# Kernel optimization log

Measured on AMD Instinct MI355X. Metric: run time of the kernel, lower is better.

The kernel has to match this reference:

```python
import jax, jax.numpy as jnp
import numpy as np

B, T, C = 4, 1024, 1024
NH, L, DHR, FF = 16, 512, 64, 4096
DK = C // NH  # 64
EPS = 1e-6
NEG = -9e15


def rms_norm(x, w):
    var = jnp.mean(jnp.square(x), axis=-1, keepdims=True)
    return x * jax.lax.rsqrt(var + EPS) * w


def rope_apply(x):
    # Faithful to RoPE module: freq = t+1, pos pairs repeated, theta = exp(-2*pos/C*ln(1e4))
    b, t, c = x.shape
    xf = x.astype(jnp.float32)
    freq = jnp.arange(t, dtype=jnp.float32)[:, None] + 1.0           # [t,1]
    pos = jnp.arange(c // 2, dtype=jnp.float32)[:, None]
    pos = jnp.repeat(pos, 2, axis=-1).reshape(1, -1)                 # [1,c] -> p0,p0,p1,p1,...
    theta = jnp.exp(-2.0 * pos / c * jnp.log(10000.0))
    cos = jnp.cos(freq * theta)                                      # [t,c]
    sin = jnp.sin(freq * theta)
    x2 = xf.reshape(b, t, c // 2, 2)
    rot = jnp.stack([-x2[..., 1], x2[..., 0]], axis=-1).reshape(b, t, c)
    return (xf * cos + rot * sin).astype(x.dtype)


def setup_inputs() -> dict:
    key = jax.random.key(0)
    ks = jax.random.split(key, 12)
    s = 0.02
    return {
        "x": jax.random.normal(ks[0], (B, T, C), jnp.float32),
        "rms1": jnp.ones((C,), jnp.float32),
        "rms2": jnp.ones((C,), jnp.float32),
        "W_dkv": s * jax.random.normal(ks[1], (C, 2 * L), jnp.float32),
        "b_dkv": jnp.zeros((2 * L,), jnp.float32),
        "W_kr": s * jax.random.normal(ks[2], (2 * L, DHR), jnp.float32),
        "b_kr": jnp.zeros((DHR,), jnp.float32),
        "W_qr": s * jax.random.normal(ks[3], (2 * L, DHR * NH), jnp.float32),
        "b_qr": jnp.zeros((DHR * NH,), jnp.float32),
        "W_kv": s * jax.random.normal(ks[4], (L, 2 * C), jnp.float32),
        "b_kv": jnp.zeros((2 * C,), jnp.float32),
        "W_q": s * jax.random.normal(ks[5], (L, C), jnp.float32),
        "b_q": jnp.zeros((C,), jnp.float32),
        "W_o": s * jax.random.normal(ks[6], (C, C), jnp.float32),
        "b_o": jnp.zeros((C,), jnp.float32),
        "W_f1": s * jax.random.normal(ks[7], (C, FF), jnp.float32),
        "b_f1": jnp.zeros((FF,), jnp.float32),
        "W_f2": s * jax.random.normal(ks[8], (FF, C), jnp.float32),
        "b_f2": jnp.zeros((C,), jnp.float32),
    }


def mla(x, W_dkv, b_dkv, W_kr, b_kr, W_qr, b_qr, W_kv, b_kv, W_q, b_q, W_o, b_o):
    b, t, c = x.shape
    comp = jnp.einsum('btc,cd->btd', x, W_dkv) + b_dkv               # [B,T,2L]
    cKV, cq = jnp.split(comp, 2, axis=-1)                            # [B,T,L] each
    # RoPE branches (computed from the compressed representation, as in source)
    kR = rope_apply(jnp.einsum('btl,ld->btd', comp, W_kr) + b_kr)    # [B,T,DHR]
    qR = rope_apply(jnp.einsum('btl,ld->btd', comp, W_qr) + b_qr)    # roped over full NH*DHR dim
    qR = qR.reshape(b, t, NH, DHR).transpose(0, 2, 1, 3)             # [B,NH,T,DHR]
    kv = jnp.einsum('btl,ld->btd', cKV, W_kv) + b_kv
    k, v = jnp.split(kv, 2, axis=-1)                                 # [B,T,C] each
    q = jnp.einsum('btl,ld->btd', cq, W_q) + b_q                     # [B,T,C]
    to_heads = lambda z: z.reshape(b, t, NH, DK).transpose(0, 2, 1, 3)
    q, k, v = to_heads(q), to_heads(k), to_heads(v)                  # [B,NH,T,DK]
    q = jnp.concatenate([q, qR], axis=-1)                            # [B,NH,T,DK+DHR]
    k = jnp.concatenate([k, jnp.broadcast_to(kR[:, None], (b, NH, t, DHR))], axis=-1)
    # manual masked softmax in fp32, scale uses DK (not DK+DHR), faithful to source
    scale = 1.0 / np.sqrt(DK)
    w = jnp.einsum('bnqd,bnkd->bnqk', q.astype(jnp.float32), k.astype(jnp.float32)) * scale
    mask = jnp.tril(jnp.ones((t, t), jnp.float32))
    w = jnp.where(mask == 0, NEG, w)
    p = jax.nn.softmax(w, axis=-1)
    o = jnp.einsum('bnqk,bnkd->bnqd', p, v.astype(jnp.float32)).astype(x.dtype)
    o = o.transpose(0, 2, 1, 3).reshape(b, t, c)
    return jnp.einsum('btc,cd->btd', o, W_o) + b_o


def ffn(x, W_f1, b_f1, W_f2, b_f2):
    h = jax.nn.gelu(jnp.einsum('btc,cf->btf', x, W_f1) + b_f1)
    return jnp.einsum('btf,fc->btc', h, W_f2) + b_f2


def reference(x, rms1, rms2, W_dkv, b_dkv, W_kr, b_kr, W_qr, b_qr,
              W_kv, b_kv, W_q, b_q, W_o, b_o, W_f1, b_f1, W_f2, b_f2):
    h = x + mla(rms_norm(x, rms1), W_dkv, b_dkv, W_kr, b_kr, W_qr, b_qr,
                W_kv, b_kv, W_q, b_q, W_o, b_o)
    out = h + ffn(rms_norm(h, rms2), W_f1, b_f1, W_f2, b_f2)
    return out
```

## Files before the change

### kernel.cpp

```cpp
#include <hip/hip_runtime.h>

typedef unsigned int u32;
typedef unsigned short u16;
typedef __bf16 bf16x8 __attribute__((ext_vector_type(8)));
typedef float f32x4 __attribute__((ext_vector_type(4)));

#define B_ 4
#define T_ 1024
#define C_ 1024
#define NH_ 16
#define L_ 512
#define DHR_ 64
#define FF_ 4096

typedef __attribute__((address_space(3))) u32 as3_u32;
typedef __attribute__((address_space(1))) u32 as1_u32;

__device__ __forceinline__ void gld16(const u16* g, u16* l) {
  __builtin_amdgcn_global_load_lds((const as1_u32*)g, (as3_u32*)l, 16, 0, 0);
}

__device__ __forceinline__ float bf2f(u16 u) {
  union { u32 i; float f; } v; v.i = ((u32)u) << 16; return v.f;
}
__device__ __forceinline__ u16 f2bf(float f) {
  union { float f; u32 i; } v; v.f = f;
  u32 r = (v.i + 0x7FFFu + ((v.i >> 16) & 1u)) >> 16;
  return (u16)r;
}

__global__ void transpose_kernel(const float* __restrict__ in, u16* __restrict__ outp,
                                 int R, int C) {
  __shared__ float tile[32][33];
  int bx = blockIdx.x * 32;
  int by = blockIdx.y * 32;
  int tx = threadIdx.x, ty = threadIdx.y;
  for (int i = ty; i < 32; i += 8)
    tile[i][tx] = in[(size_t)(by + i) * C + bx + tx];
  __syncthreads();
  for (int i = ty; i < 32; i += 8)
    outp[(size_t)(bx + i) * R + by + tx] = f2bf(tile[tx][i]);
}

__global__ __launch_bounds__(256) void rmsnorm_kernel(const float* __restrict__ xin,
                                                      const float* __restrict__ w,
                                                      u16* __restrict__ outp) {
  const int row = blockIdx.x;
  const int tid = threadIdx.x;
  const float* xp = xin + (size_t)row * C_;
  float v[4];
#pragma unroll
  for (int i = 0; i < 4; i++) v[i] = xp[tid + 256 * i];
  float ss = v[0] * v[0] + v[1] * v[1] + v[2] * v[2] + v[3] * v[3];
#pragma unroll
  for (int o = 32; o > 0; o >>= 1) ss += __shfl_down(ss, o, 64);
  __shared__ float red[4];
  if ((tid & 63) == 0) red[tid >> 6] = ss;
  __syncthreads();
  ss = red[0] + red[1] + red[2] + red[3];
  float scale = rsqrtf(ss * (1.0f / 1024.0f) + 1e-6f);
  u16* op = outp + (size_t)row * C_;
#pragma unroll
  for (int i = 0; i < 4; i++)
    op[tid + 256 * i] = f2bf(v[i] * scale * w[tid + 256 * i]);
}

template<int EPI, bool NCLIP>
__device__ __forceinline__ void g128_body(
    u16* As, u16* Bs,
    const u16* __restrict__ A, int lda, int aoff,
    const u16* __restrict__ BT, const float* __restrict__ bias,
    const float* __restrict__ resid, void* __restrict__ out,
    int N, int Kfull, int Klen, int m0, int n0, int koff) {
  const int tid = threadIdx.x;
  const int wave = tid >> 6, lane = tid & 63;
  const int wm = wave >> 1, wn = wave & 1;
  const int quad = lane >> 4, l15 = lane & 15;
  const int row = tid >> 2, seg = tid & 3;

  const u16* aP = A + (size_t)(m0 + row) * lda + aoff + koff + seg * 8;
  const u16* bP = BT + (size_t)(n0 + row) * Kfull + koff + seg * 8;
  u16* aL = As + row * 32 + seg * 8;
  u16* bL = Bs + row * 32 + seg * 8;
  const size_t aStep = (size_t)64 * lda;
  const size_t bStep = (size_t)64 * Kfull;

  f32x4 acc[4][4] = {};

  for (int k0 = 0; k0 < Klen; k0 += 32) {
    gld16(aP + k0, aL);
    gld16(aP + k0 + aStep, aL + 64 * 32);
    gld16(bP + k0, bL);
    gld16(bP + k0 + bStep, bL + 64 * 32);
    __syncthreads();
    bf16x8 af[4], bf[4];
#pragma unroll
    for (int mt = 0; mt < 4; mt++)
      af[mt] = *(const bf16x8*)&As[(wm * 64 + mt * 16 + l15) * 32 + quad * 8];
#pragma unroll
    for (int nt = 0; nt < 4; nt++)
      bf[nt] = *(const bf16x8*)&Bs[(wn * 64 + nt * 16 + l15) * 32 + quad * 8];
#pragma unroll
    for (int mt = 0; mt < 4; mt++)
#pragma unroll
      for (int nt = 0; nt < 4; nt++)
        acc[mt][nt] = __builtin_amdgcn_mfma_f32_16x16x32_bf16(af[mt], bf[nt], acc[mt][nt], 0, 0, 0);
    __syncthreads();
  }

#pragma unroll
  for (int nt = 0; nt < 4; nt++) {
    const int gn = n0 + wn * 64 + nt * 16 + l15;
    if (NCLIP && gn >= N) continue;
    const float bvv = (EPI == 4) ? 0.0f : bias[gn];
#pragma unroll
    for (int mt = 0; mt < 4; mt++) {
#pragma unroll
      for (int i = 0; i < 4; i++) {
        const int gm = m0 + wm * 64 + mt * 16 + quad * 4 + i;
        const size_t oidx = (size_t)gm * N + gn;
        float v = acc[mt][nt][i] + bvv;
        if (EPI == 2) {
          float xg = v;
          v = 0.5f * xg * (1.0f + tanhf(0.7978845608028654f * (xg + 0.044715f * xg * xg * xg)));
        }
        if (EPI == 3) v += resid[oidx];
        if (EPI == 1 || EPI == 3 || EPI == 4) ((float*)out)[oidx] = v;
        else ((u16*)out)[oidx] = f2bf(v);
      }
    }
  }
}

template<int EPI>
__global__ __launch_bounds__(256) void gemm128(
    const u16* __restrict__ A, int lda, int aoff,
    const u16* __restrict__ BT, const float* __restrict__ bias,
    const float* __restrict__ resid, void* __restrict__ out,
    int M, int N, int K) {
  __shared__ __align__(16) u16 As[128 * 32];
  __shared__ __align__(16) u16 Bs[128 * 32];
  g128_body<EPI, false>(As, Bs, A, lda, aoff, BT, bias, resid, out,
                        N, K, K, blockIdx.x * 128, blockIdx.y * 128, 0);
}

__global__ __launch_bounds__(256) void gemm128_splitk(
    const u16* __restrict__ A, int lda, const u16* __restrict__ BT,
    float* __restrict__ part, int N, int Kfull, int Klen) {
  __shared__ __align__(16) u16 As[128 * 32];
  __shared__ __align__(16) u16 Bs[128 * 32];
  const int z = blockIdx.z;
  g128_body<4, false>(As, Bs, A, lda, 0, BT, nullptr, nullptr,
                      part + (size_t)z * 4096 * N,
                      N, Kfull, Klen, blockIdx.x * 128, blockIdx.y * 128, z * Klen);
}

__global__ __launch_bounds__(256) void f2_reduce(
    const float* __restrict__ part, const float* __restrict__ h,
    const float* __restrict__ bias, float* __restrict__ out) {
  const size_t base = (size_t)blockIdx.x * 1024;
#pragma unroll
  for (int i = 0; i < 4; i++) {
    const int col = threadIdx.x + 256 * i;
    out[base + col] = h[base + col] + bias[col] + part[base + col] +
                      part[(size_t)4096 * 1024 + base + col];
  }
}

__global__ __launch_bounds__(256) void proj_fused(
    const u16* __restrict__ comp,
    const u16* __restrict__ WT_qr, const float* __restrict__ b_qr, float* __restrict__ qr_pre,
    const u16* __restrict__ WT_kr, const float* __restrict__ b_kr, float* __restrict__ kr_pre,
    const u16* __restrict__ WT_kv, const float* __restrict__ b_kv, u16* __restrict__ kvbuf,
    const u16* __restrict__ WT_q, const float* __restrict__ b_q, u16* __restrict__ qbuf) {
  __shared__ __align__(16) u16 As[128 * 32];
  __shared__ __align__(16) u16 Bs[128 * 32];
  const int m0 = blockIdx.x * 128;
  const int ny = blockIdx.y;
  if (ny < 8)
    g128_body<1, false>(As, Bs, comp, 1024, 0, WT_qr, b_qr, nullptr, qr_pre, 1024, 1024, 1024, m0, ny * 128, 0);
  else if (ny == 8)
    g128_body<1, true>(As, Bs, comp, 1024, 0, WT_kr, b_kr, nullptr, kr_pre, 64, 1024, 1024, m0, 0, 0);
  else if (ny < 25)
    g128_body<0, false>(As, Bs, comp, 1024, 0, WT_kv, b_kv, nullptr, kvbuf, 2048, 512, 512, m0, (ny - 9) * 128, 0);
  else
    g128_body<0, false>(As, Bs, comp, 1024, 512, WT_q, b_q, nullptr, qbuf, 1024, 512, 512, m0, (ny - 25) * 128, 0);
}

__global__ __launch_bounds__(256) void rope_build(
    const u16* __restrict__ qb, const float* __restrict__ qr_pre,
    const u16* __restrict__ kvb, const float* __restrict__ kr_pre,
    u16* __restrict__ Qf, u16* __restrict__ Kf) {
  const int bt = blockIdx.x;
  const int b = bt >> 10, t = bt & 1023;
  const float freq = (float)(t + 1);
  for (int idx = threadIdx.x; idx < 2048; idx += 256) {
    const int h = idx >> 7, d = idx & 127;
    const size_t dst = (((size_t)(b * 16 + h)) * T_ + t) * 128 + d;
    u16 qv, kvv;
    if (d < 64) {
      qv = qb[(size_t)bt * C_ + h * 64 + d];
      kvv = kvb[(size_t)bt * 2048 + h * 64 + d];
    } else {
      const int dd = d - 64;
      {
        const int g = h * 64 + dd;
        const int p = g >> 1;
        const float theta = __expf(-(float)(2 * p) * (9.210340372f / 1024.0f));
        float s, c;
        sincosf(freq * theta, &s, &c);
        const float x0 = qr_pre[(size_t)bt * 1024 + (p << 1)];
        const float x1 = qr_pre[(size_t)bt * 1024 + (p << 1) + 1];
        qv = f2bf((g & 1) ? (x1 * c + x0 * s) : (x0 * c - x1 * s));
      }
      {
        const int p = dd >> 1;
        const float theta = __expf(-(float)(2 * p) * (9.210340372f / 64.0f));
        float s, c;
        sincosf(freq * theta, &s, &c);
        const float x0 = kr_pre[(size_t)bt * 64 + (p << 1)];
        const float x1 = kr_pre[(size_t)bt * 64 + (p << 1) + 1];
        kvv = f2bf((dd & 1) ? (x1 * c + x0 * s) : (x0 * c - x1 * s));
      }
    }
    Qf[dst] = qv;
    Kf[dst] = kvv;
  }
}

__global__ __launch_bounds__(256) void vtrans_kernel(
    const u16* __restrict__ kvb, u16* __restrict__ Vf) {
  __shared__ u16 tile[64][72];
  const int bh = blockIdx.x, t0 = blockIdx.y * 64;
  const int b = bh >> 4, h = bh & 15;
  const int r = threadIdx.x >> 2, seg = (threadIdx.x & 3) * 16;
  const u16* src = &kvb[((size_t)(b * 1024) + t0 + r) * 2048 + 1024 + h * 64 + seg];
  *(uint4*)&tile[r][seg] = *(const uint4*)src;
  *(uint4*)&tile[r][seg + 8] = *(const uint4*)(src + 8);
  __syncthreads();
  const int d = threadIdx.x >> 2, ts = (threadIdx.x & 3) * 16;
  u16 tmp[16];
#pragma unroll
  for (int j = 0; j < 16; j++) tmp[j] = tile[ts + j][d];
  u16* dst = &Vf[((size_t)bh * 64 + d) * 1024 + t0 + ts];
  *(uint4*)dst = *(uint4*)tmp;
  *(uint4*)(dst + 8) = *(uint4*)(tmp + 8);
}

#define KSTR 136
#define VSTR 72

__global__ __launch_bounds__(256) void attn_mfma(
    const u16* __restrict__ Qf, const u16* __restrict__ Kf,
    const u16* __restrict__ Vf, u16* __restrict__ attn_o) {
  __shared__ __align__(16) u16 Ks[64 * KSTR];
  __shared__ __align__(16) u16 Vt[64 * VSTR];
  __shared__ __align__(16) u16 Ps[4][16 * VSTR];

  const int tid = threadIdx.x;
  const int wave = tid >> 6, lane = tid & 63;
  const int quad = lane >> 4, l15 = lane & 15;
  const int qt = blockIdx.x & 15;
  const int h = (blockIdx.x >> 4) & 15;
  const int b = blockIdx.x >> 8;
  const int q0 = qt * 64;
  const size_t bh = (size_t)(b * 16 + h);

  bf16x8 qfrag[4];
  {
    const u16* qb = &Qf[(bh * T_ + q0 + wave * 16 + l15) * 128 + quad * 8];
#pragma unroll
    for (int kc = 0; kc < 4; kc++) qfrag[kc] = *(const bf16x8*)(qb + kc * 32);
  }

  f32x4 acc_o[4] = {};
  float m_i[4], l_i[4];
#pragma unroll
  for (int i = 0; i < 4; i++) { m_i[i] = -3.0e38f; l_i[i] = 0.0f; }

  const int kr_ = tid >> 3, kcs = (tid & 7) * 16;
  const int vd = tid >> 2, vts = (tid & 3) * 16;

  for (int kt = 0; kt <= qt; kt++) {
    __syncthreads();
    {
      const u16* s0 = &Kf[(bh * T_ + kt * 64 + kr_) * 128 + kcs];
      const u16* s1 = s0 + 32 * 128;
      *(uint4*)&Ks[kr_ * KSTR + kcs] = *(const uint4*)s0;
      *(uint4*)&Ks[kr_ * KSTR + kcs + 8] = *(const uint4*)(s0 + 8);
      *(uint4*)&Ks[(kr_ + 32) * KSTR + kcs] = *(const uint4*)s1;
      *(uint4*)&Ks[(kr_ + 32) * KSTR + kcs + 8] = *(const uint4*)(s1 + 8);
      const u16* vs = &Vf[(bh * 64 + vd) * 1024 + kt * 64 + vts];
      *(uint4*)&Vt[vd * VSTR + vts] = *(const uint4*)vs;
      *(uint4*)&Vt[vd * VSTR + vts + 8] = *(const uint4*)(vs + 8);
    }
    __syncthreads();

    f32x4 acc_s[4] = {};
#pragma unroll
    for (int kc = 0; kc < 4; kc++) {
#pragma unroll
      for (int ng = 0; ng < 4; ng++) {
        bf16x8 bb = *(const bf16x8*)&Ks[(ng * 16 + l15) * KSTR + kc * 32 + quad * 8];
        acc_s[ng] = __builtin_amdgcn_mfma_f32_16x16x32_bf16(qfrag[kc], bb, acc_s[ng], 0, 0, 0);
      }
    }

    float sv[4][4];
#pragma unroll
    for (int ng = 0; ng < 4; ng++)
#pragma unroll
      for (int i = 0; i < 4; i++) {
        float s = acc_s[ng][i] * 0.125f;
        if (kt == qt && (ng * 16 + l15) > (wave * 16 + quad * 4 + i)) s = -3.0e38f;
        sv[ng][i] = s;
      }

    float alpha[4], mx[4];
#pragma unroll
    for (int i = 0; i < 4; i++) {
      float m = fmaxf(fmaxf(sv[0][i], sv[1][i]), fmaxf(sv[2][i], sv[3][i]));
#pragma unroll
      for (int off = 1; off < 16; off <<= 1) m = fmaxf(m, __shfl_xor(m, off, 64));
      float mn = fmaxf(m_i[i], m);
      alpha[i] = __expf(m_i[i] - mn);
      m_i[i] = mn;
      mx[i] = mn;
    }
    float rs[4] = {0.f, 0.f, 0.f, 0.f};
#pragma unroll
    for (int ng = 0; ng < 4; ng++)
#pragma unroll
      for (int i = 0; i < 4; i++) {
        float p = __expf(sv[ng][i] - mx[i]);
        rs[i] += p;
        Ps[wave][(quad * 4 + i) * VSTR + ng * 16 + l15] = f2bf(p);
      }
#pragma unroll
    for (int i = 0; i < 4; i++) {
      float r = rs[i];
#pragma unroll
      for (int off = 1; off < 16; off <<= 1) r += __shfl_xor(r, off, 64);
      l_i[i] = l_i[i] * alpha[i] + r;
    }

#pragma unroll
    for (int ng = 0; ng < 4; ng++)
#pragma unroll
      for (int i = 0; i < 4; i++) acc_o[ng][i] *= alpha[i];
#pragma unroll
    for (int kc = 0; kc < 2; kc++) {
      bf16x8 a = *(const bf16x8*)&Ps[wave][l15 * VSTR + kc * 32 + quad * 8];
#pragma unroll
      for (int ng = 0; ng < 4; ng++) {
        bf16x8 bb = *(const bf16x8*)&Vt[(ng * 16 + l15) * VSTR + kc * 32 + quad * 8];
        acc_o[ng] = __builtin_amdgcn_mfma_f32_16x16x32_bf16(a, bb, acc_o[ng], 0, 0, 0);
      }
    }
  }

  float linv[4];
#pragma unroll
  for (int i = 0; i < 4; i++) linv[i] = 1.0f / l_i[i];
#pragma unroll
  for (int ng = 0; ng < 4; ng++)
#pragma unroll
    for (int i = 0; i < 4; i++) {
      const int qrow = q0 + wave * 16 + quad * 4 + i;
      attn_o[((size_t)(b * T_) + qrow) * C_ + h * 64 + ng * 16 + l15] =
          f2bf(acc_o[ng][i] * linv[i]);
    }
}

extern "C" void kernel_launch(void* const* d_in, const int* in_sizes, int n_in,
                              void* d_out, int out_size, void* d_ws, size_t ws_size,
                              hipStream_t stream) {
  const float* x = (const float*)d_in[0];
  const float* rms1 = (const float*)d_in[1];
  const float* rms2 = (const float*)d_in[2];
  const float* W_dkv = (const float*)d_in[3];
  const float* b_dkv = (const float*)d_in[4];
  const float* W_kr = (const float*)d_in[5];
  const float* b_kr = (const float*)d_in[6];
  const float* W_qr = (const float*)d_in[7];
  const float* b_qr = (const float*)d_in[8];
  const float* W_kv = (const float*)d_in[9];
  const float* b_kv = (const float*)d_in[10];
  const float* W_q = (const float*)d_in[11];
  const float* b_q = (const float*)d_in[12];
  const float* W_o = (const float*)d_in[13];
  const float* b_o = (const float*)d_in[14];
  const float* W_f1 = (const float*)d_in[15];
  const float* b_f1 = (const float*)d_in[16];
  const float* W_f2 = (const float*)d_in[17];
  const float* b_f2 = (const float*)d_in[18];
  float* out = (float*)d_out;

  char* ws = (char*)d_ws;
  size_t off = 0;
  auto alloc = [&](size_t bytes) -> void* {
    void* p = ws + off;
    off += (bytes + 255) & ~(size_t)255;
    return p;
  };
  u16* WT_dkv = (u16*)alloc((size_t)1024 * 1024 * 2);
  u16* WT_kr  = (u16*)alloc((size_t)128 * 1024 * 2);
  u16* WT_qr  = (u16*)alloc((size_t)1024 * 1024 * 2);
  u16* WT_kv  = (u16*)alloc((size_t)2048 * 512 * 2);
  u16* WT_q   = (u16*)alloc((size_t)1024 * 512 * 2);
  u16* WT_o   = (u16*)alloc((size_t)1024 * 1024 * 2);
  u16* WT_f1  = (u16*)alloc((size_t)4096 * 1024 * 2);
  u16* WT_f2  = (u16*)alloc((size_t)1024 * 4096 * 2);
  u16* xn1    = (u16*)alloc((size_t)4096 * 1024 * 2);
  u16* comp   = (u16*)alloc((size_t)4096 * 1024 * 2);
  float* kr_pre = (float*)alloc((size_t)4096 * 64 * 4);
  float* qr_pre = (float*)alloc((size_t)4096 * 1024 * 4);
  u16* kvbuf  = (u16*)alloc((size_t)4096 * 2048 * 2);
  u16* qbuf   = (u16*)alloc((size_t)4096 * 1024 * 2);
  u16* Qf     = (u16*)alloc((size_t)64 * 1024 * 128 * 2);
  u16* Kf     = (u16*)alloc((size_t)64 * 1024 * 128 * 2);
  u16* Vf     = (u16*)alloc((size_t)64 * 64 * 1024 * 2);
  u16* attn_o = (u16*)alloc((size_t)4096 * 1024 * 2);
  float* hbuf = (float*)alloc((size_t)4096 * 1024 * 4);
  u16* hn     = (u16*)alloc((size_t)4096 * 1024 * 2);
  u16* hid    = (u16*)alloc((size_t)4096 * 4096 * 2);
  float* partial = (float*)Qf;

  dim3 tb(32, 8);
  transpose_kernel<<<dim3(32, 32), tb, 0, stream>>>(W_dkv, WT_dkv, 1024, 1024);
  transpose_kernel<<<dim3(2, 32), tb, 0, stream>>>(W_kr, WT_kr, 1024, 64);
  transpose_kernel<<<dim3(32, 32), tb, 0, stream>>>(W_qr, WT_qr, 1024, 1024);
  transpose_kernel<<<dim3(64, 16), tb, 0, stream>>>(W_kv, WT_kv, 512, 2048);
  transpose_kernel<<<dim3(32, 16), tb, 0, stream>>>(W_q, WT_q, 512, 1024);
  transpose_kernel<<<dim3(32, 32), tb, 0, stream>>>(W_o, WT_o, 1024, 1024);
  transpose_kernel<<<dim3(128, 32), tb, 0, stream>>>(W_f1, WT_f1, 1024, 4096);
  transpose_kernel<<<dim3(32, 128), tb, 0, stream>>>(W_f2, WT_f2, 4096, 1024);

  rmsnorm_kernel<<<4096, 256, 0, stream>>>(x, rms1, xn1);

  gemm128<0><<<dim3(32, 8), 256, 0, stream>>>(xn1, 1024, 0, WT_dkv, b_dkv, nullptr, comp, 4096, 1024, 1024);

  proj_fused<<<dim3(32, 33), 256, 0, stream>>>(comp,
      WT_qr, b_qr, qr_pre, WT_kr, b_kr, kr_pre,
      WT_kv, b_kv, kvbuf, WT_q, b_q, qbuf);

  rope_build<<<4096, 256, 0, stream>>>(qbuf, qr_pre, kvbuf, kr_pre, Qf, Kf);
  vtrans_kernel<<<dim3(64, 16), 256, 0, stream>>>(kvbuf, Vf);

  attn_mfma<<<B_ * NH_ * (T_ / 64), 256, 0, stream>>>(Qf, Kf, Vf, attn_o);

  gemm128<3><<<dim3(32, 8), 256, 0, stream>>>(attn_o, 1024, 0, WT_o, b_o, x, hbuf, 4096, 1024, 1024);

  rmsnorm_kernel<<<4096, 256, 0, stream>>>(hbuf, rms2, hn);

  gemm128<2><<<dim3(32, 32), 256, 0, stream>>>(hn, 1024, 0, WT_f1, b_f1, nullptr, hid, 4096, 4096, 1024);

  gemm128_splitk<<<dim3(32, 8, 2), 256, 0, stream>>>(hid, 4096, WT_f2, partial, 1024, 4096, 2048);
  f2_reduce<<<4096, 256, 0, stream>>>(partial, hbuf, b_f2, out);
}
```

Baseline: 500.4 us.

## Batch weight transposes, pair causal attention tiles, raise FFN2 split-K to four

Merges the eight weight-transpose launches into one kernel driven by a per-matrix block table, removing launch overhead. Attention blocks now process a long and a short causal query tile together (15-j and j), so per-block work is balanced and the grid is halved. The second FFN GEMM uses four K splits instead of two, with a spacer allocation so the larger partial buffer does not overlap hbuf; this raises parallelism but adds reduction traffic.

```diff
diff --git a/kernel.cpp b/kernel.cpp
--- a/kernel.cpp
+++ b/kernel.cpp
@@ -29,12 +29,27 @@
   return (u16)r;
 }
 
-__global__ void transpose_kernel(const float* __restrict__ in, u16* __restrict__ outp,
-                                 int R, int C) {
+struct TransArgs {
+  const float* src[8];
+  u16* dst[8];
+  int R[8], C[8];
+  int base[9];
+};
+
+__global__ void transpose_all(TransArgs ta) {
   __shared__ float tile[32][33];
-  int bx = blockIdx.x * 32;
-  int by = blockIdx.y * 32;
-  int tx = threadIdx.x, ty = threadIdx.y;
+  const int bid = blockIdx.x;
+  int w = 0;
+#pragma unroll
+  for (int i = 1; i < 8; i++) w += (bid >= ta.base[i]);
+  const int local = bid - ta.base[w];
+  const int R = ta.R[w], C = ta.C[w];
+  const int ctiles = C >> 5;
+  const int bx = (local % ctiles) * 32;
+  const int by = (local / ctiles) * 32;
+  const float* in = ta.src[w];
+  u16* outp = ta.dst[w];
+  const int tx = threadIdx.x, ty = threadIdx.y;
   for (int i = ty; i < 32; i += 8)
     tile[i][tx] = in[(size_t)(by + i) * C + bx + tx];
   __syncthreads();
@@ -159,11 +174,13 @@
     const float* __restrict__ part, const float* __restrict__ h,
     const float* __restrict__ bias, float* __restrict__ out) {
   const size_t base = (size_t)blockIdx.x * 1024;
+  const size_t PS = (size_t)4096 * 1024;
 #pragma unroll
   for (int i = 0; i < 4; i++) {
     const int col = threadIdx.x + 256 * i;
     out[base + col] = h[base + col] + bias[col] + part[base + col] +
-                      part[(size_t)4096 * 1024 + base + col];
+                      part[PS + base + col] + part[2 * PS + base + col] +
+                      part[3 * PS + base + col];
   }
 }
 
@@ -250,19 +267,14 @@
 #define KSTR 136
 #define VSTR 72
 
-__global__ __launch_bounds__(256) void attn_mfma(
+__device__ __forceinline__ void attn_tile(
+    u16* Ks, u16* Vt, u16* Ps,
     const u16* __restrict__ Qf, const u16* __restrict__ Kf,
-    const u16* __restrict__ Vf, u16* __restrict__ attn_o) {
-  __shared__ __align__(16) u16 Ks[64 * KSTR];
-  __shared__ __align__(16) u16 Vt[64 * VSTR];
-  __shared__ __align__(16) u16 Ps[4][16 * VSTR];
-
+    const u16* __restrict__ Vf, u16* __restrict__ attn_o,
+    int b, int h, int qt) {
   const int tid = threadIdx.x;
   const int wave = tid >> 6, lane = tid & 63;
   const int quad = lane >> 4, l15 = lane & 15;
-  const int qt = blockIdx.x & 15;
-  const int h = (blockIdx.x >> 4) & 15;
-  const int b = blockIdx.x >> 8;
   const int q0 = qt * 64;
   const size_t bh = (size_t)(b * 16 + h);
 
@@ -280,6 +292,7 @@
 
   const int kr_ = tid >> 3, kcs = (tid & 7) * 16;
   const int vd = tid >> 2, vts = (tid & 3) * 16;
+  u16* Pw = Ps + wave * 16 * VSTR;
 
   for (int kt = 0; kt <= qt; kt++) {
     __syncthreads();
@@ -334,7 +347,7 @@
       for (int i = 0; i < 4; i++) {
         float p = __expf(sv[ng][i] - mx[i]);
         rs[i] += p;
-        Ps[wave][(quad * 4 + i) * VSTR + ng * 16 + l15] = f2bf(p);
+        Pw[(quad * 4 + i) * VSTR + ng * 16 + l15] = f2bf(p);
       }
 #pragma unroll
     for (int i = 0; i < 4; i++) {
@@ -350,7 +363,7 @@
       for (int i = 0; i < 4; i++) acc_o[ng][i] *= alpha[i];
 #pragma unroll
     for (int kc = 0; kc < 2; kc++) {
-      bf16x8 a = *(const bf16x8*)&Ps[wave][l15 * VSTR + kc * 32 + quad * 8];
+      bf16x8 a = *(const bf16x8*)&Pw[l15 * VSTR + kc * 32 + quad * 8];
 #pragma unroll
       for (int ng = 0; ng < 4; ng++) {
         bf16x8 bb = *(const bf16x8*)&Vt[(ng * 16 + l15) * VSTR + kc * 32 + quad * 8];
@@ -370,6 +383,19 @@
       attn_o[((size_t)(b * T_) + qrow) * C_ + h * 64 + ng * 16 + l15] =
           f2bf(acc_o[ng][i] * linv[i]);
     }
+}
+
+__global__ __launch_bounds__(256) void attn_mfma(
+    const u16* __restrict__ Qf, const u16* __restrict__ Kf,
+    const u16* __restrict__ Vf, u16* __restrict__ attn_o) {
+  __shared__ __align__(16) u16 Ks[64 * KSTR];
+  __shared__ __align__(16) u16 Vt[64 * VSTR];
+  __shared__ __align__(16) u16 Ps[4 * 16 * VSTR];
+  const int j = blockIdx.x & 7;
+  const int h = (blockIdx.x >> 3) & 15;
+  const int b = blockIdx.x >> 7;
+  attn_tile(Ks, Vt, Ps, Qf, Kf, Vf, attn_o, b, h, 15 - j);
+  attn_tile(Ks, Vt, Ps, Qf, Kf, Vf, attn_o, b, h, j);
 }
 
 extern "C" void kernel_launch(void* const* d_in, const int* in_sizes, int n_in,
@@ -421,20 +447,25 @@
   u16* Kf     = (u16*)alloc((size_t)64 * 1024 * 128 * 2);
   u16* Vf     = (u16*)alloc((size_t)64 * 64 * 1024 * 2);
   u16* attn_o = (u16*)alloc((size_t)4096 * 1024 * 2);
+  alloc((size_t)4096 * 1024 * 4);
   float* hbuf = (float*)alloc((size_t)4096 * 1024 * 4);
   u16* hn     = (u16*)alloc((size_t)4096 * 1024 * 2);
   u16* hid    = (u16*)alloc((size_t)4096 * 4096 * 2);
   float* partial = (float*)Qf;
 
-  dim3 tb(32, 8);
-  transpose_kernel<<<dim3(32, 32), tb, 0, stream>>>(W_dkv, WT_dkv, 1024, 1024);
-  transpose_kernel<<<dim3(2, 32), tb, 0, stream>>>(W_kr, WT_kr, 1024, 64);
-  transpose_kernel<<<dim3(32, 32), tb, 0, stream>>>(W_qr, WT_qr, 1024, 1024);
-  transpose_kernel<<<dim3(64, 16), tb, 0, stream>>>(W_kv, WT_kv, 512, 2048);
-  transpose_kernel<<<dim3(32, 16), tb, 0, stream>>>(W_q, WT_q, 512, 1024);
-  transpose_kernel<<<dim3(32, 32), tb, 0, stream>>>(W_o, WT_o, 1024, 1024);
-  transpose_kernel<<<dim3(128, 32), tb, 0, stream>>>(W_f1, WT_f1, 1024, 4096);
-  transpose_kernel<<<dim3(32, 128), tb, 0, stream>>>(W_f2, WT_f2, 4096, 1024);
+  TransArgs ta;
+  const float* srcs[8] = {W_dkv, W_kr, W_qr, W_kv, W_q, W_o, W_f1, W_f2};
+  u16* dsts[8] = {WT_dkv, WT_kr, WT_qr, WT_kv, WT_q, WT_o, WT_f1, WT_f2};
+  const int Rs[8] = {1024, 1024, 1024, 512, 512, 1024, 1024, 4096};
+  const int Cs[8] = {1024, 64, 1024, 2048, 1024, 1024, 4096, 1024};
+  int acc_t = 0;
+  for (int i = 0; i < 8; i++) {
+    ta.src[i] = srcs[i]; ta.dst[i] = dsts[i]; ta.R[i] = Rs[i]; ta.C[i] = Cs[i];
+    ta.base[i] = acc_t;
+    acc_t += (Rs[i] >> 5) * (Cs[i] >> 5);
+  }
+  ta.base[8] = acc_t;
+  transpose_all<<<acc_t, dim3(32, 8), 0, stream>>>(ta);
 
   rmsnorm_kernel<<<4096, 256, 0, stream>>>(x, rms1, xn1);
 
@@ -447,7 +478,7 @@
   rope_build<<<4096, 256, 0, stream>>>(qbuf, qr_pre, kvbuf, kr_pre, Qf, Kf);
   vtrans_kernel<<<dim3(64, 16), 256, 0, stream>>>(kvbuf, Vf);
 
-  attn_mfma<<<B_ * NH_ * (T_ / 64), 256, 0, stream>>>(Qf, Kf, Vf, attn_o);
+  attn_mfma<<<B_ * NH_ * 8, 256, 0, stream>>>(Qf, Kf, Vf, attn_o);
 
   gemm128<3><<<dim3(32, 8), 256, 0, stream>>>(attn_o, 1024, 0, WT_o, b_o, x, hbuf, 4096, 1024, 1024);
 
@@ -455,6 +486,6 @@
 
   gemm128<2><<<dim3(32, 32), 256, 0, stream>>>(hn, 1024, 0, WT_f1, b_f1, nullptr, hid, 4096, 4096, 1024);
 
-  gemm128_splitk<<<dim3(32, 8, 2), 256, 0, stream>>>(hid, 4096, WT_f2, partial, 1024, 4096, 2048);
+  gemm128_splitk<<<dim3(32, 8, 4), 256, 0, stream>>>(hid, 4096, WT_f2, partial, 1024, 4096, 1024);
   f2_reduce<<<4096, 256, 0, stream>>>(partial, hbuf, b_f2, out);
 }
```

After: 471.5 us. 5.8% less time.
